# Kernel tuning notes

Measured on AMD Instinct MI355X. Metric: run time of the kernel, lower is better.

## Reference

```python
import math
import jax, jax.numpy as jnp
import numpy as np

B, W_LEN, C = 4, 2048, 768
H = 3  # fixed number of heads in the module
K = C // H  # head dim


def setup_inputs() -> dict:
    key = jax.random.key(0)
    k1, k2, k3 = jax.random.split(key, 3)
    in_sequence_bwc = jax.random.normal(k1, (B, W_LEN, C), dtype=jnp.float32)
    # torch nn.Linear weights: [out_features, in_features], scaled for stability
    W_qkv = jax.random.normal(k2, (3 * C, C), dtype=jnp.float32) * (1.0 / math.sqrt(C))
    W_proj = jax.random.normal(k3, (C, C), dtype=jnp.float32) * (1.0 / math.sqrt(C))
    return {"in_sequence_bwc": in_sequence_bwc, "W_qkv": W_qkv, "W_proj": W_proj}


def reference(in_sequence_bwc, W_qkv, W_proj):
    batch, words, coords = in_sequence_bwc.shape
    head_dim = coords // H
    # qkv projection: x @ W^T  -> [b, w, 3c]
    all_bwd = jnp.einsum("bwc,dc->bwd", in_sequence_bwc, W_qkv)
    q_bwc, k_bwc, v_bwc = jnp.split(all_bwd, 3, axis=-1)
    # [b, h, w, k]
    q = q_bwc.reshape(batch, words, H, head_dim).transpose(0, 2, 1, 3)
    k = k_bwc.reshape(batch, words, H, head_dim).transpose(0, 2, 1, 3)
    v = v_bwc.reshape(batch, words, H, head_dim).transpose(0, 2, 1, 3)
    # scaled scores with causal mask -> softmax -> @V
    scores = jnp.einsum("bhqk,bhmk->bhqm", q, k) / math.sqrt(head_dim)
    causal = jnp.tril(jnp.ones((words, words), dtype=bool))
    scores = jnp.where(causal[None, None], scores, -jnp.inf)
    probs = jax.nn.softmax(scores, axis=-1)
    out = jnp.einsum("bhqm,bhmk->bhqk", probs, v)
    out_bwc = out.transpose(0, 2, 1, 3).reshape(batch, words, coords)
    return jnp.einsum("bwc,dc->bwd", out_bwc, W_proj)
```

## Files before the change

### kernel.cpp

```cpp
#include <hip/hip_runtime.h>

using v8h = __attribute__((ext_vector_type(8))) _Float16;
using v4f = __attribute__((ext_vector_type(4))) float;
using v4u = __attribute__((ext_vector_type(4))) unsigned short;
using v8u = __attribute__((ext_vector_type(8))) unsigned short;

__device__ __forceinline__ unsigned short f2h(float x) {
  _Float16 h = (_Float16)x;
  return __builtin_bit_cast(unsigned short, h);
}
__device__ __forceinline__ float h2f(unsigned short u) {
  return (float)__builtin_bit_cast(_Float16, u);
}

__device__ __forceinline__ void gl_lds16(const unsigned short* g, unsigned short* l) {
  __builtin_amdgcn_global_load_lds(
      (const __attribute__((address_space(1))) unsigned int*)g,
      (__attribute__((address_space(3))) unsigned int*)l, 16, 0, 0);
}

__global__ void cvt3_kernel(const float* __restrict__ X,
                            const float* __restrict__ Wq,
                            const float* __restrict__ Wp,
                            unsigned short* __restrict__ Xb,
                            unsigned short* __restrict__ Wqb,
                            unsigned short* __restrict__ Wpb) {
  const int blk = (int)blockIdx.x;
  const float* src;
  unsigned short* dst;
  int i;
  if (blk < 3072)      { src = X;  dst = Xb;  i = blk * 256 + threadIdx.x; }
  else if (blk < 3936) { src = Wq; dst = Wqb; i = (blk - 3072) * 256 + threadIdx.x; }
  else                 { src = Wp; dst = Wpb; i = (blk - 3936) * 256 + threadIdx.x; }
  const float* p = src + (size_t)i * 8;
  float4 a = *(const float4*)p;
  float4 b = *(const float4*)(p + 4);
  v8u o = {f2h(a.x), f2h(a.y), f2h(a.z), f2h(a.w),
           f2h(b.x), f2h(b.y), f2h(b.z), f2h(b.w)};
  *(v8u*)(dst + (size_t)i * 8) = o;
}

__global__ __launch_bounds__(512, 2)
void qkv8_kernel(const unsigned short* __restrict__ A,
                 const unsigned short* __restrict__ Bw,
                 unsigned short* __restrict__ QK) {
  __shared__ unsigned short sm[65536];
  const int t    = (int)threadIdx.x;
  const int ln   = t & 63;
  const int wv   = t >> 6;
  const int quad = ln >> 4;
  const int L    = ln & 15;
  const int wm   = wv >> 2;
  const int wn   = wv & 3;
  const long m0  = (long)blockIdx.y * 256;
  const long n0  = (long)blockIdx.x * 256;

  const int srow = t >> 3;
  const int scol = ((t & 7) ^ (srow & 7)) * 8;
  const unsigned short* Ath = A + (m0 + srow) * 768 + scol;
  const unsigned short* Bth = Bw + (n0 + srow) * 768 + scol;
  unsigned short* lth = &sm[t * 8];

  const int l7   = L & 7;
  const int sl0  = ((0 + quad) ^ l7) * 8;
  const int sl1  = ((4 + quad) ^ l7) * 8;
  const int arow = (wm * 128 + L) * 64;
  const int brow = (wn * 64 + L) * 64;

  v4f acc[8][4];
#pragma unroll
  for (int i = 0; i < 8; i++)
#pragma unroll
    for (int j = 0; j < 4; j++) acc[i][j] = (v4f){0.f, 0.f, 0.f, 0.f};

  auto stA = [&](int tile, int h) {
    if (tile >= 12) return;
    const unsigned short* g = Ath + (h * 128) * 768 + tile * 64;
    unsigned short* l = lth + (tile & 1) * 32768 + h * 8192;
    gl_lds16(g, l);
    gl_lds16(g + 64 * 768, l + 4096);
  };
  auto stB = [&](int tile, int h) {
    if (tile >= 12) return;
    const unsigned short* g = Bth + (h * 128) * 768 + tile * 64;
    unsigned short* l = lth + (tile & 1) * 32768 + 16384 + h * 8192;
    gl_lds16(g, l);
    gl_lds16(g + 64 * 768, l + 4096);
  };

  stB(0, 0); stB(0, 1); stA(0, 0); stA(0, 1);
  stB(1, 0); stB(1, 1); stA(1, 0);
  asm volatile("s_waitcnt vmcnt(6)" ::: "memory");
  __builtin_amdgcn_s_barrier();
  __builtin_amdgcn_sched_barrier(0);

#pragma unroll 2
  for (int kt = 0; kt < 12; ++kt) {
    const unsigned short* sA = &sm[(kt & 1) * 32768];
    const unsigned short* sB = sA + 16384;
    v8h af[4][2], b0[2][2], b1[2][2];

#pragma unroll
    for (int i = 0; i < 4; i++) {
      af[i][0] = *(const v8h*)&sA[arow + i * 1024 + sl0];
      af[i][1] = *(const v8h*)&sA[arow + i * 1024 + sl1];
    }
#pragma unroll
    for (int j = 0; j < 2; j++) {
      b0[j][0] = *(const v8h*)&sB[brow + j * 1024 + sl0];
      b0[j][1] = *(const v8h*)&sB[brow + j * 1024 + sl1];
    }
    stA(kt + 1, 1);
    __builtin_amdgcn_s_barrier();
    asm volatile("s_waitcnt lgkmcnt(0)" ::: "memory");
    __builtin_amdgcn_sched_barrier(0);
    __builtin_amdgcn_s_setprio(1);
#pragma unroll
    for (int i = 0; i < 4; i++)
#pragma unroll
      for (int j = 0; j < 2; j++) {
        acc[i][j] = __builtin_amdgcn_mfma_f32_16x16x32_f16(af[i][0], b0[j][0], acc[i][j], 0, 0, 0);
        acc[i][j] = __builtin_amdgcn_mfma_f32_16x16x32_f16(af[i][1], b0[j][1], acc[i][j], 0, 0, 0);
      }
    __builtin_amdgcn_s_setprio(0);
    __builtin_amdgcn_s_barrier();
    __builtin_amdgcn_sched_barrier(0);

#pragma unroll
    for (int j = 0; j < 2; j++) {
      b1[j][0] = *(const v8h*)&sB[brow + 2048 + j * 1024 + sl0];
      b1[j][1] = *(const v8h*)&sB[brow + 2048 + j * 1024 + sl1];
    }
    __builtin_amdgcn_s_barrier();
    asm volatile("s_waitcnt lgkmcnt(0)" ::: "memory");
    __builtin_amdgcn_sched_barrier(0);
    __builtin_amdgcn_s_setprio(1);
#pragma unroll
    for (int i = 0; i < 4; i++)
#pragma unroll
      for (int j = 0; j < 2; j++) {
        acc[i][2 + j] = __builtin_amdgcn_mfma_f32_16x16x32_f16(af[i][0], b1[j][0], acc[i][2 + j], 0, 0, 0);
        acc[i][2 + j] = __builtin_amdgcn_mfma_f32_16x16x32_f16(af[i][1], b1[j][1], acc[i][2 + j], 0, 0, 0);
      }
    __builtin_amdgcn_s_setprio(0);
    __builtin_amdgcn_s_barrier();
    __builtin_amdgcn_sched_barrier(0);

#pragma unroll
    for (int i = 0; i < 4; i++) {
      af[i][0] = *(const v8h*)&sA[arow + 4096 + i * 1024 + sl0];
      af[i][1] = *(const v8h*)&sA[arow + 4096 + i * 1024 + sl1];
    }
    stB(kt + 2, 0);
    __builtin_amdgcn_s_barrier();
    asm volatile("s_waitcnt lgkmcnt(0)" ::: "memory");
    __builtin_amdgcn_sched_barrier(0);
    __builtin_amdgcn_s_setprio(1);
#pragma unroll
    for (int i = 0; i < 4; i++)
#pragma unroll
      for (int j = 0; j < 2; j++) {
        acc[4 + i][2 + j] = __builtin_amdgcn_mfma_f32_16x16x32_f16(af[i][0], b1[j][0], acc[4 + i][2 + j], 0, 0, 0);
        acc[4 + i][2 + j] = __builtin_amdgcn_mfma_f32_16x16x32_f16(af[i][1], b1[j][1], acc[4 + i][2 + j], 0, 0, 0);
      }
    __builtin_amdgcn_s_setprio(0);
    __builtin_amdgcn_s_barrier();
    __builtin_amdgcn_sched_barrier(0);

    stB(kt + 2, 1);
    stA(kt + 2, 0);
    __builtin_amdgcn_s_barrier();
    __builtin_amdgcn_sched_barrier(0);
    __builtin_amdgcn_s_setprio(1);
#pragma unroll
    for (int i = 0; i < 4; i++)
#pragma unroll
      for (int j = 0; j < 2; j++) {
        acc[4 + i][j] = __builtin_amdgcn_mfma_f32_16x16x32_f16(af[i][0], b0[j][0], acc[4 + i][j], 0, 0, 0);
        acc[4 + i][j] = __builtin_amdgcn_mfma_f32_16x16x32_f16(af[i][1], b0[j][1], acc[4 + i][j], 0, 0, 0);
      }
    __builtin_amdgcn_s_setprio(0);
    if (kt + 2 < 12)      { asm volatile("s_waitcnt vmcnt(6)" ::: "memory"); }
    else if (kt + 1 < 12) { asm volatile("s_waitcnt vmcnt(0)" ::: "memory"); }
    __builtin_amdgcn_s_barrier();
    __builtin_amdgcn_sched_barrier(0);
  }

#pragma unroll
  for (int mi = 0; mi < 8; mi++) {
    const long row = m0 + wm * 128 + (mi >> 2) * 64 + (mi & 3) * 16 + quad * 4;
#pragma unroll
    for (int nj = 0; nj < 4; nj++) {
      const long col = n0 + wn * 64 + nj * 16 + L;
#pragma unroll
      for (int r = 0; r < 4; r++)
        QK[(row + r) * 1536 + col] = f2h(acc[mi][nj][r]);
    }
  }
}

__global__ __launch_bounds__(512, 2)
void scv8_kernel(const unsigned short* __restrict__ QK,
                 const unsigned short* __restrict__ Xb,
                 const unsigned short* __restrict__ Wq,
                 unsigned short* __restrict__ Sc,
                 unsigned short* __restrict__ VT) {
  __shared__ unsigned short sm[65536];
  const int t    = (int)threadIdx.x;
  const int ln   = t & 63;
  const int wv   = t >> 6;
  const int quad = ln >> 4;
  const int L    = ln & 15;
  const int wm   = wv >> 2;
  const int wn   = wv & 3;

  const int x = (int)blockIdx.x;
  const bool isV = (x < 96);
  int NT, Ihi = 0, Jhi = 0, bh = 0, mt = 0, nt = 0;
  const unsigned short* Abase;
  const unsigned short* Bbase;
  long astr, bstr;

  if (isV) {
    mt = x & 31;
    nt = x >> 5;
    Abase = Xb + (long)mt * 256 * 768;
    Bbase = Wq + (long)(1536 + nt * 256) * 768;
    astr = 768; bstr = 768; NT = 12;
  } else {
    int s = x - 96;
    bh = s / 36;
    int slot = s % 36;
    while (slot >= Ihi + 1) { slot -= Ihi + 1; Ihi++; }
    Jhi = slot;
    const int b = bh / 3, h = bh % 3;
    Abase = QK + ((long)b * 2048 + Ihi * 256) * 1536 + h * 256;
    Bbase = QK + ((long)b * 2048 + Jhi * 256) * 1536 + 768 + h * 256;
    astr = 1536; bstr = 1536; NT = 4;
  }

  const int srow = t >> 3;
  const int scol = ((t & 7) ^ (srow & 7)) * 8;
  const unsigned short* Ath = Abase + (long)srow * astr + scol;
  const unsigned short* Bth = Bbase + (long)srow * bstr + scol;
  unsigned short* lth = &sm[t * 8];

  const int l7   = L & 7;
  const int sl0  = ((0 + quad) ^ l7) * 8;
  const int sl1  = ((4 + quad) ^ l7) * 8;
  const int arow = (wm * 128 + L) * 64;
  const int brow = (wn * 64 + L) * 64;

  v4f acc[8][4];
#pragma unroll
  for (int i = 0; i < 8; i++)
#pragma unroll
    for (int j = 0; j < 4; j++) acc[i][j] = (v4f){0.f, 0.f, 0.f, 0.f};

  auto stA = [&](int tile, int h) {
    if (tile >= NT) return;
    const unsigned short* g = Ath + (long)(h * 128) * astr + tile * 64;
    unsigned short* l = lth + (tile & 1) * 32768 + h * 8192;
    gl_lds16(g, l);
    gl_lds16(g + 64 * astr, l + 4096);
  };
  auto stB = [&](int tile, int h) {
    if (tile >= NT) return;
    const unsigned short* g = Bth + (long)(h * 128) * bstr + tile * 64;
    unsigned short* l = lth + (tile & 1) * 32768 + 16384 + h * 8192;
    gl_lds16(g, l);
    gl_lds16(g + 64 * bstr, l + 4096);
  };

  stB(0, 0); stB(0, 1); stA(0, 0); stA(0, 1);
  stB(1, 0); stB(1, 1); stA(1, 0);
  asm volatile("s_waitcnt vmcnt(6)" ::: "memory");
  __builtin_amdgcn_s_barrier();
  __builtin_amdgcn_sched_barrier(0);

#pragma unroll 2
  for (int kt = 0; kt < NT; ++kt) {
    const unsigned short* sA = &sm[(kt & 1) * 32768];
    const unsigned short* sB = sA + 16384;
    v8h af[4][2], b0[2][2], b1[2][2];

#pragma unroll
    for (int i = 0; i < 4; i++) {
      af[i][0] = *(const v8h*)&sA[arow + i * 1024 + sl0];
      af[i][1] = *(const v8h*)&sA[arow + i * 1024 + sl1];
    }
#pragma unroll
    for (int j = 0; j < 2; j++) {
      b0[j][0] = *(const v8h*)&sB[brow + j * 1024 + sl0];
      b0[j][1] = *(const v8h*)&sB[brow + j * 1024 + sl1];
    }
    stA(kt + 1, 1);
    __builtin_amdgcn_s_barrier();
    asm volatile("s_waitcnt lgkmcnt(0)" ::: "memory");
    __builtin_amdgcn_sched_barrier(0);
    __builtin_amdgcn_s_setprio(1);
#pragma unroll
    for (int i = 0; i < 4; i++)
#pragma unroll
      for (int j = 0; j < 2; j++) {
        acc[i][j] = __builtin_amdgcn_mfma_f32_16x16x32_f16(af[i][0], b0[j][0], acc[i][j], 0, 0, 0);
        acc[i][j] = __builtin_amdgcn_mfma_f32_16x16x32_f16(af[i][1], b0[j][1], acc[i][j], 0, 0, 0);
      }
    __builtin_amdgcn_s_setprio(0);
    __builtin_amdgcn_s_barrier();
    __builtin_amdgcn_sched_barrier(0);

#pragma unroll
    for (int j = 0; j < 2; j++) {
      b1[j][0] = *(const v8h*)&sB[brow + 2048 + j * 1024 + sl0];
      b1[j][1] = *(const v8h*)&sB[brow + 2048 + j * 1024 + sl1];
    }
    __builtin_amdgcn_s_barrier();
    asm volatile("s_waitcnt lgkmcnt(0)" ::: "memory");
    __builtin_amdgcn_sched_barrier(0);
    __builtin_amdgcn_s_setprio(1);
#pragma unroll
    for (int i = 0; i < 4; i++)
#pragma unroll
      for (int j = 0; j < 2; j++) {
        acc[i][2 + j] = __builtin_amdgcn_mfma_f32_16x16x32_f16(af[i][0], b1[j][0], acc[i][2 + j], 0, 0, 0);
        acc[i][2 + j] = __builtin_amdgcn_mfma_f32_16x16x32_f16(af[i][1], b1[j][1], acc[i][2 + j], 0, 0, 0);
      }
    __builtin_amdgcn_s_setprio(0);
    __builtin_amdgcn_s_barrier();
    __builtin_amdgcn_sched_barrier(0);

#pragma unroll
    for (int i = 0; i < 4; i++) {
      af[i][0] = *(const v8h*)&sA[arow + 4096 + i * 1024 + sl0];
      af[i][1] = *(const v8h*)&sA[arow + 4096 + i * 1024 + sl1];
    }
    stB(kt + 2, 0);
    __builtin_amdgcn_s_barrier();
    asm volatile("s_waitcnt lgkmcnt(0)" ::: "memory");
    __builtin_amdgcn_sched_barrier(0);
    __builtin_amdgcn_s_setprio(1);
#pragma unroll
    for (int i = 0; i < 4; i++)
#pragma unroll
      for (int j = 0; j < 2; j++) {
        acc[4 + i][2 + j] = __builtin_amdgcn_mfma_f32_16x16x32_f16(af[i][0], b1[j][0], acc[4 + i][2 + j], 0, 0, 0);
        acc[4 + i][2 + j] = __builtin_amdgcn_mfma_f32_16x16x32_f16(af[i][1], b1[j][1], acc[4 + i][2 + j], 0, 0, 0);
      }
    __builtin_amdgcn_s_setprio(0);
    __builtin_amdgcn_s_barrier();
    __builtin_amdgcn_sched_barrier(0);

    stB(kt + 2, 1);
    stA(kt + 2, 0);
    __builtin_amdgcn_s_barrier();
    __builtin_amdgcn_sched_barrier(0);
    __builtin_amdgcn_s_setprio(1);
#pragma unroll
    for (int i = 0; i < 4; i++)
#pragma unroll
      for (int j = 0; j < 2; j++) {
        acc[4 + i][j] = __builtin_amdgcn_mfma_f32_16x16x32_f16(af[i][0], b0[j][0], acc[4 + i][j], 0, 0, 0);
        acc[4 + i][j] = __builtin_amdgcn_mfma_f32_16x16x32_f16(af[i][1], b0[j][1], acc[4 + i][j], 0, 0, 0);
      }
    __builtin_amdgcn_s_setprio(0);
    if (kt + 2 < NT)      { asm volatile("s_waitcnt vmcnt(6)" ::: "memory"); }
    else if (kt + 1 < NT) { asm volatile("s_waitcnt vmcnt(0)" ::: "memory"); }
    __builtin_amdgcn_s_barrier();
    __builtin_amdgcn_sched_barrier(0);
  }

  if (isV) {
#pragma unroll
    for (int mi = 0; mi < 8; mi++) {
      const long token = (long)mt * 256 + wm * 128 + (mi >> 2) * 64 + (mi & 3) * 16 + quad * 4;
      const int b  = (int)(token >> 11);
      const int tk = (int)(token & 2047);
#pragma unroll
      for (int nj = 0; nj < 4; nj++) {
        const int colp = nt * 256 + wn * 64 + nj * 16 + L;
        const int h    = colp >> 8;
        const int d    = colp & 255;
        v4u val = {f2h(acc[mi][nj][0]), f2h(acc[mi][nj][1]),
                   f2h(acc[mi][nj][2]), f2h(acc[mi][nj][3])};
        *(v4u*)(&VT[((long)(b * 3 + h) * 256 + d) * 2048 + tk]) = val;
      }
    }
  } else {
    const int di = wm;
    const int dj = wn >> 1;
    const int i128 = 2 * Ihi + di;
    const int j128 = 2 * Jhi + dj;
    if (j128 <= i128) {
      unsigned short* Sb = Sc + ((long)bh * 136 + (long)i128 * (i128 + 1) / 2 + j128) * 16384;
#pragma unroll
      for (int mi = 0; mi < 8; mi++) {
        const int subrow = (mi >> 2) * 64 + (mi & 3) * 16 + quad * 4;
#pragma unroll
        for (int nj = 0; nj < 4; nj++) {
          const int subcol = (wn & 1) * 64 + nj * 16 + L;
#pragma unroll
          for (int r = 0; r < 4; r++)
            Sb[(subrow + r) * 128 + subcol] = f2h(acc[mi][nj][r]);
        }
      }
    }
  }
}

__global__ __launch_bounds__(512, 1)
void pvf_kernel(const unsigned short* __restrict__ Sc,
                const unsigned short* __restrict__ VT,
                unsigned short* __restrict__ AO) {
  __shared__ unsigned short sm[36864];
  __shared__ float fbuf[128];

  const int t    = (int)threadIdx.x;
  const int ln   = t & 63;
  const int wv   = t >> 6;
  const int quad = ln >> 4;
  const int L    = ln & 15;

  const int p  = (int)blockIdx.x >> 1;
  const int nh = (int)blockIdx.x & 1;
  const int bh = (int)blockIdx.y;
  const int b  = bh / 3, h = bh % 3;

  const unsigned short* VTb = VT + ((long)(bh * 256 + nh * 128)) * 2048;
  const int rloc = wv * 16 + L;

  auto stageV = [&](int jj, unsigned short* base) {
#pragma unroll
    for (int pp = 0; pp < 4; pp++) {
      const int sidx = pp * 512 + t;
      const int d    = sidx >> 4;
      const int ph   = sidx & 15;
      gl_lds16(VTb + (long)d * 2048 + jj * 128 + ((ph ^ (d & 7)) * 8),
               base + sidx * 8);
    }
  };

  for (int sel = 0; sel < 2; ++sel) {
    const int i = sel ? (15 - p) : p;
    const long Sbase = ((long)bh * 136 + (long)i * (i + 1) / 2) * 16384;

    v4f acc[8];
#pragma unroll
    for (int n = 0; n < 8; n++) acc[n] = (v4f){0.f, 0.f, 0.f, 0.f};
    float m_run = -1e30f, l_run = 0.f;

    v8u s_cur[4], s_nxt[4];
    {
      const unsigned short* Sp = Sc + Sbase + (long)rloc * 128;
#pragma unroll
      for (int ks = 0; ks < 4; ks++)
        s_cur[ks] = *(const v8u*)(Sp + ks * 32 + quad * 8);
      __builtin_amdgcn_sched_barrier(0);
      stageV(0, &sm[0]);
      __builtin_amdgcn_sched_barrier(0);
    }

    for (int j = 0; j <= i; ++j) {
      const int jn = (j < i) ? (j + 1) : i;
      const bool clamped = (j == i);
      {
        const unsigned short* Sp = Sc + Sbase + (long)jn * 16384 + (long)rloc * 128;
#pragma unroll
        for (int ks = 0; ks < 4; ks++)
          s_nxt[ks] = *(const v8u*)(Sp + ks * 32 + quad * 8);
      }
      __builtin_amdgcn_sched_barrier(0);
      if (clamped) {
#pragma unroll
        for (int pp = 0; pp < 4; pp++) {
          const int sidx = pp * 512 + t;
          const int d    = sidx >> 4;
          const int ph   = sidx & 15;
          gl_lds16(VTb + (long)d * 2048 + jn * 128 + ((ph ^ (d & 7)) * 8),
                   &sm[32768 + t * 8]);
        }
      } else {
        stageV(jn, &sm[(jn & 1) * 16384]);
      }
      __builtin_amdgcn_sched_barrier(0);

      float pv[4][8];
      float mx = -1e30f;
      if (j == i) {
#pragma unroll
        for (int ks = 0; ks < 4; ks++)
#pragma unroll
          for (int e = 0; e < 8; e++) {
            const bool valid = (ks * 32 + quad * 8 + e) <= rloc;
            const float f = valid ? h2f(s_cur[ks][e]) * 0.0625f : -1e30f;
            pv[ks][e] = f;
            mx = fmaxf(mx, f);
          }
      } else {
#pragma unroll
        for (int ks = 0; ks < 4; ks++)
#pragma unroll
          for (int e = 0; e < 8; e++) {
            const float f = h2f(s_cur[ks][e]) * 0.0625f;
            pv[ks][e] = f;
            mx = fmaxf(mx, f);
          }
      }
      mx = fmaxf(mx, __shfl_xor(mx, 16));
      mx = fmaxf(mx, __shfl_xor(mx, 32));
      const float m_new = fmaxf(m_run, mx);
      const float alpha = __expf(m_run - m_new);
      m_run = m_new;

      float sum = 0.f;
      v8h pa[4];
#pragma unroll
      for (int ks = 0; ks < 4; ks++) {
        v8h ph16;
#pragma unroll
        for (int e = 0; e < 8; e++) {
          const float pe = __expf(pv[ks][e] - m_new);
          sum += pe;
          ph16[e] = (_Float16)pe;
        }
        pa[ks] = ph16;
      }
      sum += __shfl_xor(sum, 16);
      sum += __shfl_xor(sum, 32);
      l_run = l_run * alpha + sum;

      if (quad == 0) fbuf[wv * 16 + L] = alpha;
      asm volatile("s_waitcnt lgkmcnt(0)" ::: "memory");
      __builtin_amdgcn_sched_barrier(0);
      const float a0 = fbuf[wv * 16 + quad * 4 + 0];
      const float a1 = fbuf[wv * 16 + quad * 4 + 1];
      const float a2 = fbuf[wv * 16 + quad * 4 + 2];
      const float a3 = fbuf[wv * 16 + quad * 4 + 3];
#pragma unroll
      for (int n = 0; n < 8; n++) {
        acc[n][0] *= a0; acc[n][1] *= a1; acc[n][2] *= a2; acc[n][3] *= a3;
      }

      asm volatile("s_waitcnt vmcnt(8)" ::: "memory");
      __builtin_amdgcn_s_barrier();
      __builtin_amdgcn_sched_barrier(0);

      const unsigned short* vb = &sm[(j & 1) * 16384];
      const int dx = L & 7;
#pragma unroll
      for (int nfc = 0; nfc < 8; nfc++) {
        const int dbase = (nfc * 16 + L) * 128;
        v8h v0 = *(const v8h*)&vb[dbase + ((0 + quad) ^ dx) * 8];
        v8h v1 = *(const v8h*)&vb[dbase + ((4 + quad) ^ dx) * 8];
        v8h v2 = *(const v8h*)&vb[dbase + ((8 + quad) ^ dx) * 8];
        v8h v3 = *(const v8h*)&vb[dbase + ((12 + quad) ^ dx) * 8];
        acc[nfc] = __builtin_amdgcn_mfma_f32_16x16x32_f16(pa[0], v0, acc[nfc], 0, 0, 0);
        acc[nfc] = __builtin_amdgcn_mfma_f32_16x16x32_f16(pa[1], v1, acc[nfc], 0, 0, 0);
        acc[nfc] = __builtin_amdgcn_mfma_f32_16x16x32_f16(pa[2], v2, acc[nfc], 0, 0, 0);
        acc[nfc] = __builtin_amdgcn_mfma_f32_16x16x32_f16(pa[3], v3, acc[nfc], 0, 0, 0);
      }
      __builtin_amdgcn_s_barrier();
      __builtin_amdgcn_sched_barrier(0);

#pragma unroll
      for (int ks = 0; ks < 4; ks++) s_cur[ks] = s_nxt[ks];
    }

    const float inv = 1.0f / l_run;
    if (quad == 0) fbuf[wv * 16 + L] = inv;
    asm volatile("s_waitcnt lgkmcnt(0)" ::: "memory");
    __builtin_amdgcn_sched_barrier(0);
    const float i0 = fbuf[wv * 16 + quad * 4 + 0];
    const float i1 = fbuf[wv * 16 + quad * 4 + 1];
    const float i2 = fbuf[wv * 16 + quad * 4 + 2];
    const float i3 = fbuf[wv * 16 + quad * 4 + 3];

    unsigned short* Ob = AO + ((long)b * 2048 + (long)i * 128 + wv * 16 + quad * 4) * 768
                            + h * 256 + nh * 128 + L;
#pragma unroll
    for (int n = 0; n < 8; n++) {
      Ob[0 * 768 + n * 16] = f2h(acc[n][0] * i0);
      Ob[1 * 768 + n * 16] = f2h(acc[n][1] * i1);
      Ob[2 * 768 + n * 16] = f2h(acc[n][2] * i2);
      Ob[3 * 768 + n * 16] = f2h(acc[n][3] * i3);
    }
    __builtin_amdgcn_s_barrier();
  }
}

__global__ __launch_bounds__(256, 2)
void gemm_proj_kernel(const unsigned short* __restrict__ A,
                      const unsigned short* __restrict__ Bw,
                      float* __restrict__ C) {
  __shared__ unsigned short As[4096];
  __shared__ unsigned short Bs[4096];

  const int t    = threadIdx.x;
  const int ln   = t & 63;
  const int wv   = t >> 6;
  const int quad = ln >> 4;
  const int L    = ln & 15;
  const int wm   = (wv >> 1) * 64;
  const int wn   = (wv & 1) * 64;
  const long m0  = (long)blockIdx.y * 128;
  const long n0  = (long)blockIdx.x * 128;

  v4f acc[4][4];
#pragma unroll
  for (int i = 0; i < 4; i++)
#pragma unroll
    for (int j = 0; j < 4; j++) acc[i][j] = (v4f){0.f, 0.f, 0.f, 0.f};

  const int ar = t >> 2;
  const int ac = (t & 3) * 8;
  const unsigned short* Ag = A + (m0 + ar) * 768 + ac;
  const unsigned short* Bg = Bw + (n0 + ar) * 768 + ac;
  unsigned short* la = &As[t * 8];
  unsigned short* lb = &Bs[t * 8];
  const long rowskip = 64L * 768;

  for (int k0 = 0; k0 < 768; k0 += 32) {
    gl_lds16(Ag + k0, la);
    gl_lds16(Ag + rowskip + k0, la + 2048);
    gl_lds16(Bg + k0, lb);
    gl_lds16(Bg + rowskip + k0, lb + 2048);
    __syncthreads();

    v8h af[4], bfr[4];
#pragma unroll
    for (int i = 0; i < 4; i++)
      af[i] = *(const v8h*)(&As[(wm + i * 16 + L) * 32 + quad * 8]);
#pragma unroll
    for (int j = 0; j < 4; j++)
      bfr[j] = *(const v8h*)(&Bs[(wn + j * 16 + L) * 32 + quad * 8]);
#pragma unroll
    for (int i = 0; i < 4; i++)
#pragma unroll
      for (int j = 0; j < 4; j++)
        acc[i][j] = __builtin_amdgcn_mfma_f32_16x16x32_f16(af[i], bfr[j], acc[i][j], 0, 0, 0);
    __syncthreads();
  }

#pragma unroll
  for (int i = 0; i < 4; i++)
#pragma unroll
    for (int j = 0; j < 4; j++)
#pragma unroll
      for (int r = 0; r < 4; r++) {
        long row = m0 + wm + i * 16 + quad * 4 + r;
        long col = n0 + wn + j * 16 + L;
        C[row * 768 + col] = acc[i][j][r];
      }
}

extern "C" void kernel_launch(void* const* d_in, const int* in_sizes, int n_in,
                              void* d_out, int out_size, void* d_ws, size_t ws_size,
                              hipStream_t stream) {
  const float* X     = (const float*)d_in[0];
  const float* Wqkv  = (const float*)d_in[1];
  const float* Wproj = (const float*)d_in[2];
  float* out = (float*)d_out;

  const size_t SZ_QK = (size_t)8192 * 1536 * 2;
  const size_t SZ_VT = (size_t)3072 * 2048 * 2;
  const size_t SZ_SC = (size_t)12 * 136 * 16384 * 2;
  const size_t SZ_AO = (size_t)8192 * 768 * 2;
  const size_t SZ_WQ = (size_t)2304 * 768 * 2;

  char* ws = (char*)d_ws;
  unsigned short* QKb = (unsigned short*)ws;
  unsigned short* VTb = (unsigned short*)(ws + SZ_QK);
  unsigned short* Scb = (unsigned short*)(ws + SZ_QK + SZ_VT);
  unsigned short* AOb = (unsigned short*)(ws + SZ_QK + SZ_VT + SZ_SC);
  unsigned short* Xb  = AOb;
  unsigned short* Wqb = (unsigned short*)(ws + SZ_QK + SZ_VT + SZ_SC + SZ_AO);
  unsigned short* Wpb = (unsigned short*)(ws + SZ_QK + SZ_VT + SZ_SC + SZ_AO + SZ_WQ);

  dim3 blk(256, 1, 1);
  cvt3_kernel<<<dim3(4224, 1, 1), blk, 0, stream>>>(X, Wqkv, Wproj, Xb, Wqb, Wpb);
  qkv8_kernel<<<dim3(6, 32, 1), dim3(512, 1, 1), 0, stream>>>(Xb, Wqb, QKb);
  scv8_kernel<<<dim3(528, 1, 1), dim3(512, 1, 1), 0, stream>>>(QKb, Xb, Wqb, Scb, VTb);
  pvf_kernel<<<dim3(16, 12, 1), dim3(512, 1, 1), 0, stream>>>(Scb, VTb, AOb);
  gemm_proj_kernel<<<dim3(6, 64, 1), blk, 0, stream>>>(AOb, Wpb, out);
}
```

Baseline: 223.6 us.

## Triple-buffer V tiles in PV kernel and skip rescale when max stable

```diff
diff --git a/kernel.cpp b/kernel.cpp
--- a/kernel.cpp
+++ b/kernel.cpp
@@ -199,6 +199,71 @@
   }
 }
 
+__global__ __launch_bounds__(256, 2)
+void gemm_proj_kernel(const unsigned short* __restrict__ A,
+                      const unsigned short* __restrict__ Bw,
+                      float* __restrict__ C) {
+  __shared__ unsigned short As[4096];
+  __shared__ unsigned short Bs[4096];
+
+  const int t    = threadIdx.x;
+  const int ln   = t & 63;
+  const int wv   = t >> 6;
+  const int quad = ln >> 4;
+  const int L    = ln & 15;
+  const int wm   = (wv >> 1) * 64;
+  const int wn   = (wv & 1) * 64;
+  const long m0  = (long)blockIdx.y * 128;
+  const long n0  = (long)blockIdx.x * 128;
+
+  v4f acc[4][4];
+#pragma unroll
+  for (int i = 0; i < 4; i++)
+#pragma unroll
+    for (int j = 0; j < 4; j++) acc[i][j] = (v4f){0.f, 0.f, 0.f, 0.f};
+
+  const int ar = t >> 2;
+  const int ac = (t & 3) * 8;
+  const unsigned short* Ag = A + (m0 + ar) * 768 + ac;
+  const unsigned short* Bg = Bw + (n0 + ar) * 768 + ac;
+  unsigned short* la = &As[t * 8];
+  unsigned short* lb = &Bs[t * 8];
+  const long rowskip = 64L * 768;
+
+  for (int k0 = 0; k0 < 768; k0 += 32) {
+    gl_lds16(Ag + k0, la);
+    gl_lds16(Ag + rowskip + k0, la + 2048);
+    gl_lds16(Bg + k0, lb);
+    gl_lds16(Bg + rowskip + k0, lb + 2048);
+    __syncthreads();
+
+    v8h af[4], bfr[4];
+#pragma unroll
+    for (int i = 0; i < 4; i++)
+      af[i] = *(const v8h*)(&As[(wm + i * 16 + L) * 32 + quad * 8]);
+#pragma unroll
+    for (int j = 0; j < 4; j++)
+      bfr[j] = *(const v8h*)(&Bs[(wn + j * 16 + L) * 32 + quad * 8]);
+#pragma unroll
+    for (int i = 0; i < 4; i++)
+#pragma unroll
+      for (int j = 0; j < 4; j++)
+        acc[i][j] = __builtin_amdgcn_mfma_f32_16x16x32_f16(af[i], bfr[j], acc[i][j], 0, 0, 0);
+    __syncthreads();
+  }
+
+#pragma unroll
+  for (int i = 0; i < 4; i++)
+#pragma unroll
+    for (int j = 0; j < 4; j++)
+#pragma unroll
+      for (int r = 0; r < 4; r++) {
+        long row = m0 + wm + i * 16 + quad * 4 + r;
+        long col = n0 + wn + j * 16 + L;
+        C[row * 768 + col] = acc[i][j][r];
+      }
+}
+
 __global__ __launch_bounds__(512, 2)
 void scv8_kernel(const unsigned short* __restrict__ QK,
                  const unsigned short* __restrict__ Xb,
@@ -412,7 +477,7 @@
 void pvf_kernel(const unsigned short* __restrict__ Sc,
                 const unsigned short* __restrict__ VT,
                 unsigned short* __restrict__ AO) {
-  __shared__ unsigned short sm[36864];
+  __shared__ unsigned short sm[49152];
   __shared__ float fbuf[128];
 
   const int t    = (int)threadIdx.x;
@@ -457,36 +522,30 @@
         s_cur[ks] = *(const v8u*)(Sp + ks * 32 + quad * 8);
       __builtin_amdgcn_sched_barrier(0);
       stageV(0, &sm[0]);
+      if (i >= 1) stageV(1, &sm[16384]);
       __builtin_amdgcn_sched_barrier(0);
     }
 
     for (int j = 0; j <= i; ++j) {
-      const int jn = (j < i) ? (j + 1) : i;
-      const bool clamped = (j == i);
-      {
-        const unsigned short* Sp = Sc + Sbase + (long)jn * 16384 + (long)rloc * 128;
+      const bool last = (j == i);
+      if (!last) {
+        const unsigned short* Sp = Sc + Sbase + (long)(j + 1) * 16384 + (long)rloc * 128;
 #pragma unroll
         for (int ks = 0; ks < 4; ks++)
           s_nxt[ks] = *(const v8u*)(Sp + ks * 32 + quad * 8);
       }
       __builtin_amdgcn_sched_barrier(0);
-      if (clamped) {
-#pragma unroll
-        for (int pp = 0; pp < 4; pp++) {
-          const int sidx = pp * 512 + t;
-          const int d    = sidx >> 4;
-          const int ph   = sidx & 15;
-          gl_lds16(VTb + (long)d * 2048 + jn * 128 + ((ph ^ (d & 7)) * 8),
-                   &sm[32768 + t * 8]);
-        }
-      } else {
-        stageV(jn, &sm[(jn & 1) * 16384]);
-      }
+      if (last)        { asm volatile("s_waitcnt vmcnt(0)" ::: "memory"); }
+      else if (j == 0) { asm volatile("s_waitcnt vmcnt(8)" ::: "memory"); }
+      else             { asm volatile("s_waitcnt vmcnt(12)" ::: "memory"); }
+      __builtin_amdgcn_s_barrier();
+      __builtin_amdgcn_sched_barrier(0);
+      if (j + 2 <= i) stageV(j + 2, &sm[((j + 2) % 3) * 16384]);
       __builtin_amdgcn_sched_barrier(0);
 
       float pv[4][8];
       float mx = -1e30f;
-      if (j == i) {
+      if (last) {
 #pragma unroll
         for (int ks = 0; ks < 4; ks++)
 #pragma unroll
@@ -508,9 +567,14 @@
       }
       mx = fmaxf(mx, __shfl_xor(mx, 16));
       mx = fmaxf(mx, __shfl_xor(mx, 32));
-      const float m_new = fmaxf(m_run, mx);
-      const float alpha = __expf(m_run - m_new);
-      m_run = m_new;
+
+      const bool keepm = __all(mx <= m_run + 8.f);
+      float alpha = 1.f;
+      if (!keepm) {
+        const float m_new = fmaxf(m_run, mx);
+        alpha = __expf(m_run - m_new);
+        m_run = m_new;
+      }
 
       float sum = 0.f;
       v8h pa[4];
@@ -519,7 +583,7 @@
         v8h ph16;
 #pragma unroll
         for (int e = 0; e < 8; e++) {
-          const float pe = __expf(pv[ks][e] - m_new);
+          const float pe = __expf(pv[ks][e] - m_run);
           sum += pe;
           ph16[e] = (_Float16)pe;
         }
@@ -527,25 +591,25 @@
       }
       sum += __shfl_xor(sum, 16);
       sum += __shfl_xor(sum, 32);
-      l_run = l_run * alpha + sum;
-
-      if (quad == 0) fbuf[wv * 16 + L] = alpha;
-      asm volatile("s_waitcnt lgkmcnt(0)" ::: "memory");
-      __builtin_amdgcn_sched_barrier(0);
-      const float a0 = fbuf[wv * 16 + quad * 4 + 0];
-      const float a1 = fbuf[wv * 16 + quad * 4 + 1];
-      const float a2 = fbuf[wv * 16 + quad * 4 + 2];
-      const float a3 = fbuf[wv * 16 + quad * 4 + 3];
-#pragma unroll
-      for (int n = 0; n < 8; n++) {
-        acc[n][0] *= a0; acc[n][1] *= a1; acc[n][2] *= a2; acc[n][3] *= a3;
-      }
-
-      asm volatile("s_waitcnt vmcnt(8)" ::: "memory");
-      __builtin_amdgcn_s_barrier();
-      __builtin_amdgcn_sched_barrier(0);
-
-      const unsigned short* vb = &sm[(j & 1) * 16384];
+
+      if (keepm) {
+        l_run = l_run + sum;
+      } else {
+        l_run = l_run * alpha + sum;
+        if (quad == 0) fbuf[wv * 16 + L] = alpha;
+        asm volatile("s_waitcnt lgkmcnt(0)" ::: "memory");
+        __builtin_amdgcn_sched_barrier(0);
+        const float a0 = fbuf[wv * 16 + quad * 4 + 0];
+        const float a1 = fbuf[wv * 16 + quad * 4 + 1];
+        const float a2 = fbuf[wv * 16 + quad * 4 + 2];
+        const float a3 = fbuf[wv * 16 + quad * 4 + 3];
+#pragma unroll
+        for (int n = 0; n < 8; n++) {
+          acc[n][0] *= a0; acc[n][1] *= a1; acc[n][2] *= a2; acc[n][3] *= a3;
+        }
+      }
+
+      const unsigned short* vb = &sm[(j % 3) * 16384];
       const int dx = L & 7;
 #pragma unroll
       for (int nfc = 0; nfc < 8; nfc++) {
@@ -559,8 +623,6 @@
         acc[nfc] = __builtin_amdgcn_mfma_f32_16x16x32_f16(pa[2], v2, acc[nfc], 0, 0, 0);
         acc[nfc] = __builtin_amdgcn_mfma_f32_16x16x32_f16(pa[3], v3, acc[nfc], 0, 0, 0);
       }
-      __builtin_amdgcn_s_barrier();
-      __builtin_amdgcn_sched_barrier(0);
 
 #pragma unroll
       for (int ks = 0; ks < 4; ks++) s_cur[ks] = s_nxt[ks];
@@ -586,71 +648,6 @@
     }
     __builtin_amdgcn_s_barrier();
   }
-}
-
-__global__ __launch_bounds__(256, 2)
-void gemm_proj_kernel(const unsigned short* __restrict__ A,
-                      const unsigned short* __restrict__ Bw,
-                      float* __restrict__ C) {
-  __shared__ unsigned short As[4096];
-  __shared__ unsigned short Bs[4096];
-
-  const int t    = threadIdx.x;
-  const int ln   = t & 63;
-  const int wv   = t >> 6;
-  const int quad = ln >> 4;
-  const int L    = ln & 15;
-  const int wm   = (wv >> 1) * 64;
-  const int wn   = (wv & 1) * 64;
-  const long m0  = (long)blockIdx.y * 128;
-  const long n0  = (long)blockIdx.x * 128;
-
-  v4f acc[4][4];
-#pragma unroll
-  for (int i = 0; i < 4; i++)
-#pragma unroll
-    for (int j = 0; j < 4; j++) acc[i][j] = (v4f){0.f, 0.f, 0.f, 0.f};
-
-  const int ar = t >> 2;
-  const int ac = (t & 3) * 8;
-  const unsigned short* Ag = A + (m0 + ar) * 768 + ac;
-  const unsigned short* Bg = Bw + (n0 + ar) * 768 + ac;
-  unsigned short* la = &As[t * 8];
-  unsigned short* lb = &Bs[t * 8];
-  const long rowskip = 64L * 768;
-
-  for (int k0 = 0; k0 < 768; k0 += 32) {
-    gl_lds16(Ag + k0, la);
-    gl_lds16(Ag + rowskip + k0, la + 2048);
-    gl_lds16(Bg + k0, lb);
-    gl_lds16(Bg + rowskip + k0, lb + 2048);
-    __syncthreads();
-
-    v8h af[4], bfr[4];
-#pragma unroll
-    for (int i = 0; i < 4; i++)
-      af[i] = *(const v8h*)(&As[(wm + i * 16 + L) * 32 + quad * 8]);
-#pragma unroll
-    for (int j = 0; j < 4; j++)
-      bfr[j] = *(const v8h*)(&Bs[(wn + j * 16 + L) * 32 + quad * 8]);
-#pragma unroll
-    for (int i = 0; i < 4; i++)
-#pragma unroll
-      for (int j = 0; j < 4; j++)
-        acc[i][j] = __builtin_amdgcn_mfma_f32_16x16x32_f16(af[i], bfr[j], acc[i][j], 0, 0, 0);
-    __syncthreads();
-  }
-
-#pragma unroll
-  for (int i = 0; i < 4; i++)
-#pragma unroll
-    for (int j = 0; j < 4; j++)
-#pragma unroll
-      for (int r = 0; r < 4; r++) {
-        long row = m0 + wm + i * 16 + quad * 4 + r;
-        long col = n0 + wn + j * 16 + L;
-        C[row * 768 + col] = acc[i][j][r];
-      }
 }
 
 extern "C" void kernel_launch(void* const* d_in, const int* in_sizes, int n_in,
```

Result: faster. 218.7 us, median of 2 (-2.2%).
